# Optimization experiments

Measured on AMD Instinct MI355X. Metric: run time of the kernel, lower is better.

## Reference

```python
import jax, jax.numpy as jnp
import numpy as np

B, S = 16, 768
DCOG, DENV, NENV = 64, 32, 8
D, N, L, FF, NC = 512, 64, 6, 2048, 1
DIL = (1, 2, 4, 8)
EPS = 1e-5


def _layer_norm(x, g, b):
    m = x.mean(-1, keepdims=True)
    v = ((x - m) ** 2).mean(-1, keepdims=True)
    return (x - m) * jax.lax.rsqrt(v + EPS) * g + b


def _conv1d(x, w, b, d):
    # x: (B, D, S), w: (O, I, K); 'same' padding = (K-1)*d//2 = d for K=3
    y = jax.lax.conv_general_dilated(x, w, (1,), [(d, d)], rhs_dilation=(d,),
                                     dimension_numbers=('NCH', 'OIH', 'NCH'))
    return y + b[None, :, None]


def _combine(c1, c2):
    a1, b1 = c1
    a2, b2 = c2
    return a1 * a2, a2 * b1 + b2


def _forward(x_cog, cw1, cb1, cw2, cb2, env_emb, ew1, eb1, ew2, eb2,
             fw1, fb1, fw2, fb2, pos_enc, conv_w, conv_b, wm_w, wm_b,
             ssm_w, ssm_b, A_log, ffw1, ffb1, ffw2, ffb2,
             g1, be1, g2, be2, pw1, pb1, pw2, pb2, x_env):
    # Dual-channel feature processor (dropout = identity at eval)
    z = x_cog / jnp.maximum(jnp.linalg.norm(x_cog, axis=-1, keepdims=True), 1e-12)
    z = jnp.maximum(z @ cw1 + cb1, 0.0) @ cw2 + cb2
    e = env_emb[x_env].mean(-2)                      # (B,S,NENV,D) -> (B,S,D)
    e = jnp.maximum(e @ ew1 + eb1, 0.0) @ ew2 + eb2
    hf = jnp.concatenate([z, e], -1)
    hf = jnp.maximum(hf @ fw1 + fb1, 0.0) @ fw2 + fb2
    h = hf + pos_enc[:S][None]

    def layer_step(h, p):
        cw, cb, wmw, wmb, sw, sb, alog, w1, b1, w2, b2, g1_, be1_, g2_, be2_ = p
        # Multi-scale dilated conv
        xt = h.transpose(0, 2, 1)                    # (B, D, S)
        outs = [_conv1d(xt, cw[i], cb[i], DIL[i]) for i in range(4)]
        alpha = jax.nn.softmax(xt.mean(-1) @ wmw + wmb, -1)   # (B, 4)
        hm = sum(alpha[:, i, None, None] * outs[i] for i in range(4)).transpose(0, 2, 1)
        h1 = _layer_norm(hm + h, g1_, be1_)
        # Selective state-space (diagonal A), parallel associative scan
        proj = jnp.einsum('bsd,kdn->kbsn', h1, sw) + sb[:, None, None, :]
        delta, Bt, Ct = jax.nn.softplus(proj[0]), proj[1], proj[2]
        a = jnp.exp(alog[None, None, :] * delta)     # (B, S, N)
        bu = Bt * h1[..., :N]
        _, hs = jax.lax.associative_scan(_combine, (a, bu), axis=1)
        y = jnp.sum(Ct * hs, -1, keepdims=True)      # (B, S, 1)
        h2 = _layer_norm(y + h1, g2_, be2_)          # broadcast over D, as in torch
        return jnp.maximum(h2 @ w1 + b1, 0.0) @ w2 + b2 + h2, None

    h, _ = jax.lax.scan(layer_step, h, (conv_w, conv_b, wm_w, wm_b, ssm_w, ssm_b,
                                        A_log, ffw1, ffb1, ffw2, ffb2, g1, be1, g2, be2))
    hg = h.mean(1)                                   # adaptive avg pool over S
    return jnp.maximum(hg @ pw1 + pb1, 0.0) @ pw2 + pb2


def setup_inputs():
    ks = iter(jax.random.split(jax.random.key(0), 48))
    def rn(shape, s=0.02):
        return jax.random.normal(next(ks), shape, jnp.float32) * s
    return {
        'x_cog': rn((B, S, DCOG), 1.0),
        'cw1': rn((DCOG, D)), 'cb1': jnp.zeros(D), 'cw2': rn((D, D)), 'cb2': jnp.zeros(D),
        'env_emb': rn((DENV, D), 1.0),
        'ew1': rn((D, D)), 'eb1': jnp.zeros(D), 'ew2': rn((D, D)), 'eb2': jnp.zeros(D),
        'fw1': rn((2 * D, D)), 'fb1': jnp.zeros(D), 'fw2': rn((D, D)), 'fb2': jnp.zeros(D),
        'pos_enc': rn((1000, D), 1.0),
        'conv_w': rn((L, 4, D, D, 3)), 'conv_b': jnp.zeros((L, 4, D)),
        'wm_w': rn((L, D, 4)), 'wm_b': jnp.zeros((L, 4)),
        'ssm_w': rn((L, 3, D, N)), 'ssm_b': jnp.zeros((L, 3, N)),
        'A_log': -jnp.abs(rn((L, N), 1.0)),
        'ffw1': rn((L, D, FF)), 'ffb1': jnp.zeros((L, FF)),
        'ffw2': rn((L, FF, D)), 'ffb2': jnp.zeros((L, D)),
        'g1': jnp.ones((L, D)), 'be1': jnp.zeros((L, D)),
        'g2': jnp.ones((L, D)), 'be2': jnp.zeros((L, D)),
        'pw1': rn((D, D // 2)), 'pb1': jnp.zeros(D // 2),
        'pw2': rn((D // 2, NC)), 'pb2': jnp.zeros(NC),
        'x_env': jax.random.randint(next(ks), (B, S, NENV), 0, DENV, jnp.int32),
    }


def reference(x_cog, cw1, cb1, cw2, cb2, env_emb, ew1, eb1, ew2, eb2,
              fw1, fb1, fw2, fb2, pos_enc, conv_w, conv_b, wm_w, wm_b,
              ssm_w, ssm_b, A_log, ffw1, ffb1, ffw2, ffb2,
              g1, be1, g2, be2, pw1, pb1, pw2, pb2, x_env):
    return _forward(x_cog, cw1, cb1, cw2, cb2, env_emb, ew1, eb1, ew2, eb2,
                    fw1, fb1, fw2, fb2, pos_enc, conv_w, conv_b, wm_w, wm_b,
                    ssm_w, ssm_b, A_log, ffw1, ffb1, ffw2, ffb2,
                    g1, be1, g2, be2, pw1, pb1, pw2, pb2, x_env)
```

## Files before the change

### kernel.cpp

```cpp
#include <hip/hip_runtime.h>
#include <cstdint>
#include <cstddef>

namespace {

constexpr int B = 16, S = 768, BS = B * S, D = 512, FF = 2048, L = 6;
constexpr float EPS = 1e-5f;

typedef float f32x4 __attribute__((ext_vector_type(4)));
typedef _Float16 f16x8 __attribute__((ext_vector_type(8)));

__device__ __forceinline__ float wave_sum(float v) {
#pragma unroll
  for (int o = 32; o > 0; o >>= 1) v += __shfl_xor(v, o, 64);
  return v;
}

__device__ __forceinline__ short f16b(float x) {
  const _Float16 h = (_Float16)x;
  return __builtin_bit_cast(short, h);
}

__device__ __forceinline__ void gload16(const void* g, void* l) {
  __builtin_amdgcn_global_load_lds(
      (const __attribute__((address_space(1))) void*)g,
      (__attribute__((address_space(3))) void*)l, 16, 0, 0);
}


template <bool RELU, bool RESID, bool FOUT, bool PACK>
__global__ __launch_bounds__(256, 3) void gemm_h(
    const short* __restrict__ A, int lda, const short* __restrict__ Wt,
    int ldw, int Klen, const float* __restrict__ bias,
    const float* __restrict__ resid, int ldr, int rmod,
    float* __restrict__ fout, int ldc, short* __restrict__ ph, int ldp) {
  __shared__ alignas(16) short sAh[8192], sBh[8192];
  const int tid = threadIdx.x;
  const unsigned Nt = gridDim.x;
  const unsigned lin = blockIdx.y * Nt + blockIdx.x;
  const unsigned cpx = (Nt * gridDim.y) >> 3;
  const unsigned swz = (lin & 7) * cpx + (lin >> 3);
  const int bn = (int)(swz % Nt) * 128, bm = (int)(swz / Nt) * 128;
  const int wave = tid >> 6, lane = tid & 63;
  const int wr = (wave >> 1) * 64, wc = (wave & 1) * 64;
  const int lr = lane & 15, sl = lane >> 4;
  const short* Ab = A + (size_t)bm * lda;
  const short* Wb = Wt + (size_t)bn * ldw;
  f32x4 acc[4][4] = {};
  for (int kk = 0; kk < Klen; kk += 64) {
#pragma unroll
    for (int jj = 0; jj < 4; ++jj) {
      const int G = jj * 256 + tid;
      const int srow = G >> 3, sl0 = G & 7;
      const int gsl = sl0 ^ (srow & 7);
      const int dst = G * 8;
      gload16(Ab + (size_t)srow * lda + kk + gsl * 8, &sAh[dst]);
      gload16(Wb + (size_t)srow * ldw + kk + gsl * 8, &sBh[dst]);
    }
    __syncthreads();
#pragma unroll
    for (int ks = 0; ks < 2; ++ks) {
      f16x8 aH[4], bH[4];
#pragma unroll
      for (int m = 0; m < 4; ++m) {
        const int r = wr + m * 16 + lr;
        aH[m] = *(const f16x8*)&sAh[r * 64 + (((ks * 4 + sl) ^ (r & 7)) * 8)];
      }
#pragma unroll
      for (int n = 0; n < 4; ++n) {
        const int r = wc + n * 16 + lr;
        bH[n] = *(const f16x8*)&sBh[r * 64 + (((ks * 4 + sl) ^ (r & 7)) * 8)];
      }
#pragma unroll
      for (int m = 0; m < 4; ++m)
#pragma unroll
        for (int n = 0; n < 4; ++n)
          acc[m][n] = __builtin_amdgcn_mfma_f32_16x16x32_f16(aH[m], bH[n],
                                                             acc[m][n], 0, 0, 0);
    }
    __syncthreads();
  }
  const int r4 = sl * 4;
#pragma unroll
  for (int m = 0; m < 4; ++m) {
#pragma unroll
    for (int r = 0; r < 4; ++r) {
      const int mm = bm + wr + m * 16 + r4 + r;
#pragma unroll
      for (int n = 0; n < 4; ++n) {
        const int col = bn + wc + n * 16 + lr;
        float v = acc[m][n][r] + bias[col];
        if (RELU) v = fmaxf(v, 0.f);
        if (RESID) {
          const int rr = rmod ? (mm % rmod) : mm;
          v += resid[(size_t)rr * ldr + col];
        }
        if (FOUT) fout[(size_t)mm * ldc + col] = v;
        if (PACK) ph[(size_t)mm * ldp + col] = f16b(v);
      }
    }
  }
}

template <bool RELU, bool RESID, bool FOUT, bool PACK>
__global__ __launch_bounds__(256, 3) void gemm_h64(
    const short* __restrict__ A, int lda, const short* __restrict__ Wt,
    int ldw, int Klen, const float* __restrict__ bias,
    const float* __restrict__ resid, int ldr, int rmod,
    float* __restrict__ fout, int ldc, short* __restrict__ ph, int ldp) {
  __shared__ alignas(16) short sAh[8192], sBh[4096];
  const int tid = threadIdx.x;
  const unsigned Nt = gridDim.x;
  const unsigned lin = blockIdx.y * Nt + blockIdx.x;
  const unsigned cpx = (Nt * gridDim.y) >> 3;
  const unsigned swz = (lin & 7) * cpx + (lin >> 3);
  const int bn = (int)(swz % Nt) * 64, bm = (int)(swz / Nt) * 128;
  const int wave = tid >> 6, lane = tid & 63;
  const int wr = (wave >> 1) * 64, wc = (wave & 1) * 32;
  const int lr = lane & 15, sl = lane >> 4;
  const short* Ab = A + (size_t)bm * lda;
  const short* Wb = Wt + (size_t)bn * ldw;
  f32x4 acc[4][2] = {};
  for (int kk = 0; kk < Klen; kk += 64) {
#pragma unroll
    for (int jj = 0; jj < 4; ++jj) {
      const int G = jj * 256 + tid;
      const int srow = G >> 3, sl0 = G & 7;
      const int gsl = sl0 ^ (srow & 7);
      gload16(Ab + (size_t)srow * lda + kk + gsl * 8, &sAh[G * 8]);
    }
#pragma unroll
    for (int jj = 0; jj < 2; ++jj) {
      const int G = jj * 256 + tid;
      const int srow = G >> 3, sl0 = G & 7;
      const int gsl = sl0 ^ (srow & 7);
      gload16(Wb + (size_t)srow * ldw + kk + gsl * 8, &sBh[G * 8]);
    }
    __syncthreads();
#pragma unroll
    for (int ks = 0; ks < 2; ++ks) {
      f16x8 aH[4], bH[2];
#pragma unroll
      for (int m = 0; m < 4; ++m) {
        const int r = wr + m * 16 + lr;
        aH[m] = *(const f16x8*)&sAh[r * 64 + (((ks * 4 + sl) ^ (r & 7)) * 8)];
      }
#pragma unroll
      for (int n = 0; n < 2; ++n) {
        const int r = wc + n * 16 + lr;
        bH[n] = *(const f16x8*)&sBh[r * 64 + (((ks * 4 + sl) ^ (r & 7)) * 8)];
      }
#pragma unroll
      for (int m = 0; m < 4; ++m)
#pragma unroll
        for (int n = 0; n < 2; ++n)
          acc[m][n] = __builtin_amdgcn_mfma_f32_16x16x32_f16(aH[m], bH[n],
                                                             acc[m][n], 0, 0, 0);
    }
    __syncthreads();
  }
  const int r4 = sl * 4;
#pragma unroll
  for (int m = 0; m < 4; ++m) {
#pragma unroll
    for (int r = 0; r < 4; ++r) {
      const int mm = bm + wr + m * 16 + r4 + r;
#pragma unroll
      for (int n = 0; n < 2; ++n) {
        const int col = bn + wc + n * 16 + lr;
        float v = acc[m][n][r] + bias[col];
        if (RELU) v = fmaxf(v, 0.f);
        if (RESID) {
          const int rr = rmod ? (mm % rmod) : mm;
          v += resid[(size_t)rr * ldr + col];
        }
        if (FOUT) fout[(size_t)mm * ldc + col] = v;
        if (PACK) ph[(size_t)mm * ldp + col] = f16b(v);
      }
    }
  }
}

__global__ __launch_bounds__(256, 3) void conv_zp_k(
    const short* __restrict__ hp, const short* __restrict__ wt8,
    const short* __restrict__ wmix, const float* __restrict__ alpha,
    const short* __restrict__ zpadS, float* __restrict__ P) {
  __shared__ alignas(16) short sAh[8192], sBh[8192];
  const int tid = threadIdx.x;
  const unsigned lin = blockIdx.x;
  const unsigned swz = (lin & 7) * 96 + (lin >> 3);
  const int zp = (int)(swz / 384);
  const unsigned rem = swz % 384;
  const int bn = (int)(rem & 3) * 128;
  const int bmt = (int)(rem >> 2);
  const int b = bmt / 6, s0 = (bmt % 6) * 128, gm0 = bmt * 128;
  const int wave = tid >> 6, lane = tid & 63;
  const int wr = (wave >> 1) * 64, wc = (wave & 1) * 64;
  const int lr = lane & 15, sl = lane >> 4;
  const short* hb = hp + (size_t)b * S * 512;
  f32x4 accF[4][4] = {};
#pragma unroll
  for (int zi = 0; zi < 2; ++zi) {
    const int z = zp * 2 + zi;
    const int dd = 1 << z;
    f32x4 acc[4][4] = {};
    for (int kk = 0; kk < 1024; kk += 64) {
      const int tap = kk >> 9;
      const int koff = kk & 511;
      const int off = tap ? dd : -dd;
#pragma unroll
      for (int jj = 0; jj < 4; ++jj) {
        const int G = jj * 256 + tid;
        const int srow = G >> 3, sl0 = G & 7;
        const int gsl = sl0 ^ (srow & 7);
        const int dst = G * 8;
        const int gs = s0 + srow + off;
        const bool inb = ((unsigned)gs < (unsigned)S);
        const short* aBase = hb + (size_t)gs * 512 + koff + gsl * 8;
        gload16(inb ? aBase : zpadS, &sAh[dst]);
        gload16(wt8 + ((size_t)((z * 2 + tap) * 512 + bn + srow)) * 512 +
                    koff + gsl * 8,
                &sBh[dst]);
      }
      __syncthreads();
#pragma unroll
      for (int ks = 0; ks < 2; ++ks) {
        f16x8 aH[4], bH[4];
#pragma unroll
        for (int m = 0; m < 4; ++m) {
          const int r = wr + m * 16 + lr;
          aH[m] =
              *(const f16x8*)&sAh[r * 64 + (((ks * 4 + sl) ^ (r & 7)) * 8)];
        }
#pragma unroll
        for (int n = 0; n < 4; ++n) {
          const int r = wc + n * 16 + lr;
          bH[n] =
              *(const f16x8*)&sBh[r * 64 + (((ks * 4 + sl) ^ (r & 7)) * 8)];
        }
#pragma unroll
        for (int m = 0; m < 4; ++m)
#pragma unroll
          for (int n = 0; n < 4; ++n)
            acc[m][n] = __builtin_amdgcn_mfma_f32_16x16x32_f16(
                aH[m], bH[n], acc[m][n], 0, 0, 0);
      }
      __syncthreads();
    }
    const float al = alpha[b * 4 + z];
#pragma unroll
    for (int m = 0; m < 4; ++m)
#pragma unroll
      for (int n = 0; n < 4; ++n)
#pragma unroll
        for (int r = 0; r < 4; ++r) accF[m][n][r] += al * acc[m][n][r];
  }
  const short* Wm = wmix + (size_t)b * 512 * 512;
  for (int kc = 0; kc < 256; kc += 64) {
    const int koff = zp * 256 + kc;
#pragma unroll
    for (int jj = 0; jj < 4; ++jj) {
      const int G = jj * 256 + tid;
      const int srow = G >> 3, sl0 = G & 7;
      const int gsl = sl0 ^ (srow & 7);
      const int dst = G * 8;
      gload16(hb + (size_t)(s0 + srow) * 512 + koff + gsl * 8, &sAh[dst]);
      gload16(Wm + (size_t)(bn + srow) * 512 + koff + gsl * 8, &sBh[dst]);
    }
    __syncthreads();
#pragma unroll
    for (int ks = 0; ks < 2; ++ks) {
      f16x8 aH[4], bH[4];
#pragma unroll
      for (int m = 0; m < 4; ++m) {
        const int r = wr + m * 16 + lr;
        aH[m] = *(const f16x8*)&sAh[r * 64 + (((ks * 4 + sl) ^ (r & 7)) * 8)];
      }
#pragma unroll
      for (int n = 0; n < 4; ++n) {
        const int r = wc + n * 16 + lr;
        bH[n] = *(const f16x8*)&sBh[r * 64 + (((ks * 4 + sl) ^ (r & 7)) * 8)];
      }
#pragma unroll
      for (int m = 0; m < 4; ++m)
#pragma unroll
        for (int n = 0; n < 4; ++n)
          accF[m][n] = __builtin_amdgcn_mfma_f32_16x16x32_f16(
              aH[m], bH[n], accF[m][n], 0, 0, 0);
    }
    __syncthreads();
  }
  float* Pz = P + (size_t)zp * ((size_t)BS * D);
  const int r4 = sl * 4;
#pragma unroll
  for (int m = 0; m < 4; ++m)
#pragma unroll
    for (int r = 0; r < 4; ++r) {
      const int mm = gm0 + wr + m * 16 + r4 + r;
#pragma unroll
      for (int n = 0; n < 4; ++n)
        Pz[(size_t)mm * D + bn + wc + n * 16 + lr] = accF[m][n][r];
    }
}

__global__ __launch_bounds__(256) void ln3_k(
    const float* __restrict__ P0, const float* __restrict__ P1,
    const float* __restrict__ resid, const float* __restrict__ cbmix,
    const float* __restrict__ g1, const float* __restrict__ b1,
    const float* __restrict__ g2, const float* __restrict__ b2,
    float* __restrict__ fout, short* __restrict__ pout) {
  const int row = blockIdx.x * 4 + (threadIdx.x >> 6);
  const int lane = threadIdx.x & 63;
  const int bb = row / S;
  const size_t base = (size_t)row * D;
  float v[8];
  float s = 0.f;
#pragma unroll
  for (int j = 0; j < 8; ++j) {
    const int c = lane + 64 * j;
    v[j] = P0[base + c] + P1[base + c] + resid[base + c] +
           cbmix[(size_t)bb * D + c];
    s += v[j];
  }
  s = wave_sum(s);
  const float m1 = s * (1.f / D);
  float q = 0.f;
#pragma unroll
  for (int j = 0; j < 8; ++j) { const float d = v[j] - m1; q += d * d; }
  q = wave_sum(q);
  const float r1 = rsqrtf(q * (1.f / D) + EPS);
  float y[8];
  float s2 = 0.f;
#pragma unroll
  for (int j = 0; j < 8; ++j) {
    const int c = lane + 64 * j;
    y[j] = (v[j] - m1) * r1 * g1[c] + b1[c];
    s2 += y[j];
  }
  s2 = wave_sum(s2);
  const float m2 = s2 * (1.f / D);
  float q2 = 0.f;
#pragma unroll
  for (int j = 0; j < 8; ++j) { const float d = y[j] - m2; q2 += d * d; }
  q2 = wave_sum(q2);
  const float r2 = rsqrtf(q2 * (1.f / D) + EPS);
  float* frow = fout + base;
  short* prow = pout + (size_t)row * 512;
#pragma unroll
  for (int j = 0; j < 8; ++j) {
    const int c = lane + 64 * j;
    const float o = (y[j] - m2) * r2 * g2[c] + b2[c];
    frow[c] = o;
    prow[c] = f16b(o);
  }
}

__global__ __launch_bounds__(256) void colmean_part_k(
    const float* __restrict__ x, float* __restrict__ part) {
  const int b = blockIdx.x, c = blockIdx.y;
  const int s0 = c * 96;
  for (int d = threadIdx.x; d < D; d += 256) {
    float s = 0.f;
    for (int si = 0; si < 96; ++si)
      s += x[((size_t)b * S + s0 + si) * D + d];
    part[((size_t)b * 8 + c) * D + d] = s;
  }
}

__global__ __launch_bounds__(256) void pack_wh_k(const float* __restrict__ W,
                                                 short* __restrict__ out,
                                                 int K, int N, int ln2N) {
  const int idx = blockIdx.x * 256 + threadIdx.x;
  const int n = idx & (N - 1), k = idx >> ln2N;
  if (k >= K) return;
  out[(size_t)n * K + k] = f16b(W[(size_t)k * N + n]);
}

__global__ __launch_bounds__(256) void pack_convw8_k(
    const float* __restrict__ cw, short* __restrict__ out) {
  const int idx = blockIdx.x * 256 + threadIdx.x;
  const int c = idx & 511, o = (idx >> 9) & 511, seg = idx >> 18;
  const int z = seg >> 1, t = (seg & 1) * 2;
  out[((size_t)seg * D + o) * D + c] =
      f16b(cw[(((size_t)z * D + o) * D + c) * 3 + t]);
}

__global__ __launch_bounds__(256) void wmix_k(const float* __restrict__ cw,
                                              const float* __restrict__ alpha,
                                              short* __restrict__ wm) {
  __shared__ float sal[64];
  if (threadIdx.x < 64) sal[threadIdx.x] = alpha[threadIdx.x];
  __syncthreads();
  const int idx = blockIdx.x * 256 + threadIdx.x;
  const int c = idx & 511, o = idx >> 9;
  float w[4];
#pragma unroll
  for (int z = 0; z < 4; ++z)
    w[z] = cw[(((size_t)z * D + o) * D + c) * 3 + 1];
#pragma unroll
  for (int b = 0; b < 16; ++b) {
    const float v = sal[b * 4 + 0] * w[0] + sal[b * 4 + 1] * w[1] +
                    sal[b * 4 + 2] * w[2] + sal[b * 4 + 3] * w[3];
    wm[((size_t)b * D + o) * D + c] = f16b(v);
  }
}

__global__ __launch_bounds__(256) void zero_k(float* __restrict__ p) {
  p[threadIdx.x] = 0.f;
  p[threadIdx.x + 256] = 0.f;
}

__global__ __launch_bounds__(64) void alpha_k(const float* __restrict__ part,
                                              const float* __restrict__ wmw,
                                              const float* __restrict__ wmb,
                                              const float* __restrict__ cb,
                                              float* __restrict__ alpha,
                                              float* __restrict__ cbmix) {
  const int b = blockIdx.x, t = threadIdx.x;
  float p0 = 0, p1 = 0, p2 = 0, p3 = 0;
  for (int d = t; d < D; d += 64) {
    float xm = 0;
#pragma unroll
    for (int c = 0; c < 8; ++c) xm += part[((size_t)b * 8 + c) * D + d];
    xm *= (1.f / S);
    p0 += xm * wmw[d * 4 + 0];
    p1 += xm * wmw[d * 4 + 1];
    p2 += xm * wmw[d * 4 + 2];
    p3 += xm * wmw[d * 4 + 3];
  }
  p0 = wave_sum(p0); p1 = wave_sum(p1);
  p2 = wave_sum(p2); p3 = wave_sum(p3);
  const float l0 = p0 + wmb[0], l1 = p1 + wmb[1];
  const float l2 = p2 + wmb[2], l3 = p3 + wmb[3];
  const float mx = fmaxf(fmaxf(l0, l1), fmaxf(l2, l3));
  const float e0 = expf(l0 - mx), e1 = expf(l1 - mx);
  const float e2 = expf(l2 - mx), e3 = expf(l3 - mx);
  const float inv = 1.f / (e0 + e1 + e2 + e3);
  const float a0 = e0 * inv, a1 = e1 * inv, a2 = e2 * inv, a3 = e3 * inv;
  if (t == 0) {
    alpha[b * 4 + 0] = a0;
    alpha[b * 4 + 1] = a1;
    alpha[b * 4 + 2] = a2;
    alpha[b * 4 + 3] = a3;
  }
  for (int c = t; c < D; c += 64)
    cbmix[(size_t)b * D + c] =
        a0 * cb[c] + a1 * cb[D + c] + a2 * cb[2 * D + c] + a3 * cb[3 * D + c];
}

__global__ __launch_bounds__(256) void embed_k(const int* __restrict__ xe,
                                               const float* __restrict__ emb,
                                               short* __restrict__ out) {
  const int r = blockIdx.x;
  int idx[8];
#pragma unroll
  for (int j = 0; j < 8; ++j) idx[j] = xe[r * 8 + j];
  short* o = out + (size_t)r * 512;
  for (int d = threadIdx.x; d < D; d += 256) {
    float s = 0.f;
#pragma unroll
    for (int j = 0; j < 8; ++j) s += emb[(size_t)idx[j] * D + d];
    o[d] = f16b(s * 0.125f);
  }
}

__global__ __launch_bounds__(256) void norml2_k(const float* __restrict__ x,
                                                short* __restrict__ out) {
  const int r = blockIdx.x * 4 + (threadIdx.x >> 6);
  const int lane = threadIdx.x & 63;
  const float v = x[(size_t)r * 64 + lane];
  const float s = wave_sum(v * v);
  const float nrm = fmaxf(sqrtf(s), 1e-12f);
  out[(size_t)r * 64 + lane] = f16b(v / nrm);
}

__global__ __launch_bounds__(256) void head_k(
    const float* __restrict__ part, const float* __restrict__ pw1,
    const float* __restrict__ pb1, const float* __restrict__ pw2,
    const float* __restrict__ pb2, float* __restrict__ out) {
  __shared__ float hg[D];
  __shared__ float red[256];
  const int b = blockIdx.x, t = threadIdx.x;
  for (int d = t; d < D; d += 256) {
    float s = 0.f;
#pragma unroll
    for (int c = 0; c < 8; ++c) s += part[((size_t)b * 8 + c) * D + d];
    hg[d] = s * (1.f / S);
  }
  __syncthreads();
  float s = pb1[t];
  for (int d = 0; d < D; ++d) s = fmaf(hg[d], pw1[(size_t)d * 256 + t], s);
  s = fmaxf(s, 0.f);
  red[t] = s * pw2[t];
  __syncthreads();
  for (int o = 128; o > 0; o >>= 1) {
    if (t < o) red[t] += red[t + o];
    __syncthreads();
  }
  if (t == 0) out[b] = red[0] + pb2[0];
}

}

extern "C" void kernel_launch(void* const* d_in, const int* in_sizes, int n_in,
                              void* d_out, int out_size, void* d_ws,
                              size_t ws_size, hipStream_t stream) {
  const float* x_cog = (const float*)d_in[0];
  const float* cw1 = (const float*)d_in[1];
  const float* cb1 = (const float*)d_in[2];
  const float* cw2 = (const float*)d_in[3];
  const float* cb2 = (const float*)d_in[4];
  const float* env_emb = (const float*)d_in[5];
  const float* ew1 = (const float*)d_in[6];
  const float* eb1 = (const float*)d_in[7];
  const float* ew2 = (const float*)d_in[8];
  const float* eb2 = (const float*)d_in[9];
  const float* fw1 = (const float*)d_in[10];
  const float* fb1 = (const float*)d_in[11];
  const float* fw2 = (const float*)d_in[12];
  const float* fb2 = (const float*)d_in[13];
  const float* pos_enc = (const float*)d_in[14];
  const float* conv_w = (const float*)d_in[15];
  const float* conv_b = (const float*)d_in[16];
  const float* wm_w = (const float*)d_in[17];
  const float* wm_b = (const float*)d_in[18];
  const float* ffw1 = (const float*)d_in[22];
  const float* ffb1 = (const float*)d_in[23];
  const float* ffw2 = (const float*)d_in[24];
  const float* ffb2 = (const float*)d_in[25];
  const float* g1 = (const float*)d_in[26];
  const float* be1 = (const float*)d_in[27];
  const float* g2 = (const float*)d_in[28];
  const float* be2 = (const float*)d_in[29];
  const float* pw1 = (const float*)d_in[30];
  const float* pb1 = (const float*)d_in[31];
  const float* pw2 = (const float*)d_in[32];
  const float* pb2 = (const float*)d_in[33];
  const int* x_env = (const int*)d_in[34];
  float* out = (float*)d_out;

  float* ws = (float*)d_ws;
  float* Hbuf = ws;
  float* TBuf = Hbuf + 6291456;
  float* PARTb = TBuf + 6291456;
  float* ALPHAB = PARTb + 65536;
  float* ZPADF = ALPHAB + 64;
  float* CBMIX = ZPADF + 512;
  short* R = (short*)(CBMIX + 8192);
  short* CONC = R;
  short* PK1 = R + 25165824;
  short* PK2 = R + 31457280;
  short* WPBF = R + 37748736;
  short* WCONV8 = R;
  short* WFFP = R + 2097152;
  short* WMIX = R + 3145728;
  float* convP = (float*)(R + 7340032);
  short* APFF = R + 7340032;
  short* HPACK = R + 57671680;

  const dim3 blk(256);
  const dim3 gS(8, 96, 1);
  const dim3 gF(16, 96, 1);

  zero_k<<<1, blk, 0, stream>>>(ZPADF);

  norml2_k<<<BS / 4, blk, 0, stream>>>(x_cog, PK1);
  pack_wh_k<<<64 * 512 / 256, blk, 0, stream>>>(cw1, WPBF, 64, 512, 9);
  gemm_h64<true, false, false, true><<<gS, blk, 0, stream>>>(
      PK1, 64, WPBF, 64, 64, cb1, nullptr, 0, 0, nullptr, 0, PK2, 512);
  pack_wh_k<<<512 * 512 / 256, blk, 0, stream>>>(cw2, WPBF, 512, 512, 9);
  gemm_h64<false, false, false, true><<<gS, blk, 0, stream>>>(
      PK2, 512, WPBF, 512, 512, cb2, nullptr, 0, 0, nullptr, 0, CONC, 2048);
  embed_k<<<BS, blk, 0, stream>>>(x_env, env_emb, PK1);
  pack_wh_k<<<512 * 512 / 256, blk, 0, stream>>>(ew1, WPBF, 512, 512, 9);
  gemm_h64<true, false, false, true><<<gS, blk, 0, stream>>>(
      PK1, 512, WPBF, 512, 512, eb1, nullptr, 0, 0, nullptr, 0, PK2, 512);
  pack_wh_k<<<512 * 512 / 256, blk, 0, stream>>>(ew2, WPBF, 512, 512, 9);
  gemm_h64<false, false, false, true><<<gS, blk, 0, stream>>>(
      PK2, 512, WPBF, 512, 512, eb2, nullptr, 0, 0, nullptr, 0, CONC + 512,
      2048);
  pack_wh_k<<<1024 * 512 / 256, blk, 0, stream>>>(fw1, WPBF, 1024, 512, 9);
  gemm_h64<true, false, false, true><<<gS, blk, 0, stream>>>(
      CONC, 2048, WPBF, 1024, 1024, fb1, nullptr, 0, 0, nullptr, 0, PK1, 512);
  pack_wh_k<<<512 * 512 / 256, blk, 0, stream>>>(fw2, WPBF, 512, 512, 9);
  gemm_h64<false, true, true, true><<<gS, blk, 0, stream>>>(
      PK1, 512, WPBF, 512, 512, fb2, pos_enc, 512, S, Hbuf, 512, HPACK, 512);

  for (int l = 0; l < L; ++l) {
    const float* cwl = conv_w + (size_t)l * 4 * D * D * 3;
    colmean_part_k<<<dim3(B, 8), blk, 0, stream>>>(Hbuf, PARTb);
    alpha_k<<<B, dim3(64), 0, stream>>>(PARTb, wm_w + (size_t)l * D * 4,
                                        wm_b + l * 4,
                                        conv_b + (size_t)l * 4 * D, ALPHAB,
                                        CBMIX);
    wmix_k<<<1024, blk, 0, stream>>>(cwl, ALPHAB, WMIX);
    pack_convw8_k<<<8 * 512 * 512 / 256, blk, 0, stream>>>(cwl, WCONV8);
    conv_zp_k<<<768, blk, 0, stream>>>(HPACK, WCONV8, WMIX, ALPHAB,
                                       (const short*)ZPADF, convP);
    ln3_k<<<BS / 4, blk, 0, stream>>>(convP, convP + 6291456, Hbuf, CBMIX,
                                      g1 + l * D, be1 + l * D, g2 + l * D,
                                      be2 + l * D, TBuf, HPACK);
    pack_wh_k<<<512 * 2048 / 256, blk, 0, stream>>>(ffw1 + (size_t)l * D * FF,
                                                    WFFP, 512, 2048, 11);
    gemm_h<true, false, false, true><<<gF, blk, 0, stream>>>(
        HPACK, 512, WFFP, 512, 512, ffb1 + (size_t)l * FF, nullptr, 0, 0,
        nullptr, 0, APFF, 2048);
    pack_wh_k<<<2048 * 512 / 256, blk, 0, stream>>>(ffw2 + (size_t)l * FF * D,
                                                    WFFP, 2048, 512, 9);
    gemm_h64<false, true, true, true><<<gS, blk, 0, stream>>>(
        APFF, 2048, WFFP, 2048, 2048, ffb2 + (size_t)l * D, TBuf, 512, 0,
        Hbuf, 512, HPACK, 512);
  }

  colmean_part_k<<<dim3(B, 8), blk, 0, stream>>>(Hbuf, PARTb);
  head_k<<<B, blk, 0, stream>>>(PARTb, pw1, pb1, pw2, pb2, out);
}
```

Before: 1.376 ms.

## Fuse column sums into GEMM epilogue, fp16 conv partials, tiled weight packing

The separate colmean kernel is removed. The D-dimension column sums of each 128-row tile are now produced in the epilogue of the FF2/fusion GEMMs, and alpha/head read 6 partials per batch. The conv partial outputs are stored as fp16 instead of fp32, halving that round-trip traffic at some precision cost. Weight transposition now goes through an LDS tile so both reads and writes are coalesced. The two conv weight prep kernels are merged into one launch, and the workspace layout is reshuffled to fit.

```diff
diff --git a/kernel.cpp b/kernel.cpp
--- a/kernel.cpp
+++ b/kernel.cpp
@@ -19,6 +19,9 @@
 __device__ __forceinline__ short f16b(float x) {
   const _Float16 h = (_Float16)x;
   return __builtin_bit_cast(short, h);
+}
+__device__ __forceinline__ float h2f(short s) {
+  return (float)__builtin_bit_cast(_Float16, s);
 }
 
 __device__ __forceinline__ void gload16(const void* g, void* l) {
@@ -102,19 +105,22 @@
   }
 }
 
-template <bool RELU, bool RESID, bool FOUT, bool PACK>
+template <bool RELU, bool RESID, bool FOUT, bool PACK, bool CSUM>
 __global__ __launch_bounds__(256, 3) void gemm_h64(
     const short* __restrict__ A, int lda, const short* __restrict__ Wt,
     int ldw, int Klen, const float* __restrict__ bias,
     const float* __restrict__ resid, int ldr, int rmod,
-    float* __restrict__ fout, int ldc, short* __restrict__ ph, int ldp) {
+    float* __restrict__ fout, int ldc, short* __restrict__ ph, int ldp,
+    float* __restrict__ part) {
   __shared__ alignas(16) short sAh[8192], sBh[4096];
+  __shared__ float csLds[2][64];
   const int tid = threadIdx.x;
   const unsigned Nt = gridDim.x;
   const unsigned lin = blockIdx.y * Nt + blockIdx.x;
   const unsigned cpx = (Nt * gridDim.y) >> 3;
   const unsigned swz = (lin & 7) * cpx + (lin >> 3);
-  const int bn = (int)(swz % Nt) * 64, bm = (int)(swz / Nt) * 128;
+  const int bn = (int)(swz % Nt) * 64, bmt = (int)(swz / Nt);
+  const int bm = bmt * 128;
   const int wave = tid >> 6, lane = tid & 63;
   const int wr = (wave >> 1) * 64, wc = (wave & 1) * 32;
   const int lr = lane & 15, sl = lane >> 4;
@@ -160,6 +166,7 @@
     __syncthreads();
   }
   const int r4 = sl * 4;
+  float cs[2] = {0.f, 0.f};
 #pragma unroll
   for (int m = 0; m < 4; ++m) {
 #pragma unroll
@@ -176,15 +183,30 @@
         }
         if (FOUT) fout[(size_t)mm * ldc + col] = v;
         if (PACK) ph[(size_t)mm * ldp + col] = f16b(v);
-      }
-    }
+        if (CSUM) cs[n] += v;
+      }
+    }
+  }
+  if constexpr (CSUM) {
+#pragma unroll
+    for (int n = 0; n < 2; ++n) {
+      cs[n] += __shfl_xor(cs[n], 16, 64);
+      cs[n] += __shfl_xor(cs[n], 32, 64);
+    }
+    if (sl == 0) {
+      csLds[wave >> 1][wc + lr] = cs[0];
+      csLds[wave >> 1][wc + 16 + lr] = cs[1];
+    }
+    __syncthreads();
+    if (tid < 64)
+      part[(size_t)bmt * 512 + bn + tid] = csLds[0][tid] + csLds[1][tid];
   }
 }
 
 __global__ __launch_bounds__(256, 3) void conv_zp_k(
     const short* __restrict__ hp, const short* __restrict__ wt8,
     const short* __restrict__ wmix, const float* __restrict__ alpha,
-    const short* __restrict__ zpadS, float* __restrict__ P) {
+    const short* __restrict__ zpadS, short* __restrict__ P) {
   __shared__ alignas(16) short sAh[8192], sBh[8192];
   const int tid = threadIdx.x;
   const unsigned lin = blockIdx.x;
@@ -290,7 +312,7 @@
     }
     __syncthreads();
   }
-  float* Pz = P + (size_t)zp * ((size_t)BS * D);
+  short* Pz = P + (size_t)zp * ((size_t)BS * D);
   const int r4 = sl * 4;
 #pragma unroll
   for (int m = 0; m < 4; ++m)
@@ -299,12 +321,12 @@
       const int mm = gm0 + wr + m * 16 + r4 + r;
 #pragma unroll
       for (int n = 0; n < 4; ++n)
-        Pz[(size_t)mm * D + bn + wc + n * 16 + lr] = accF[m][n][r];
+        Pz[(size_t)mm * D + bn + wc + n * 16 + lr] = f16b(accF[m][n][r]);
     }
 }
 
 __global__ __launch_bounds__(256) void ln3_k(
-    const float* __restrict__ P0, const float* __restrict__ P1,
+    const short* __restrict__ P0, const short* __restrict__ P1,
     const float* __restrict__ resid, const float* __restrict__ cbmix,
     const float* __restrict__ g1, const float* __restrict__ b1,
     const float* __restrict__ g2, const float* __restrict__ b2,
@@ -318,7 +340,7 @@
 #pragma unroll
   for (int j = 0; j < 8; ++j) {
     const int c = lane + 64 * j;
-    v[j] = P0[base + c] + P1[base + c] + resid[base + c] +
+    v[j] = h2f(P0[base + c]) + h2f(P1[base + c]) + resid[base + c] +
            cbmix[(size_t)bb * D + c];
     s += v[j];
   }
@@ -355,53 +377,51 @@
   }
 }
 
-__global__ __launch_bounds__(256) void colmean_part_k(
-    const float* __restrict__ x, float* __restrict__ part) {
-  const int b = blockIdx.x, c = blockIdx.y;
-  const int s0 = c * 96;
-  for (int d = threadIdx.x; d < D; d += 256) {
-    float s = 0.f;
-    for (int si = 0; si < 96; ++si)
-      s += x[((size_t)b * S + s0 + si) * D + d];
-    part[((size_t)b * 8 + c) * D + d] = s;
-  }
-}
-
-__global__ __launch_bounds__(256) void pack_wh_k(const float* __restrict__ W,
+__global__ __launch_bounds__(256) void pack_wt_k(const float* __restrict__ W,
                                                  short* __restrict__ out,
-                                                 int K, int N, int ln2N) {
-  const int idx = blockIdx.x * 256 + threadIdx.x;
-  const int n = idx & (N - 1), k = idx >> ln2N;
-  if (k >= K) return;
-  out[(size_t)n * K + k] = f16b(W[(size_t)k * N + n]);
-}
-
-__global__ __launch_bounds__(256) void pack_convw8_k(
-    const float* __restrict__ cw, short* __restrict__ out) {
-  const int idx = blockIdx.x * 256 + threadIdx.x;
-  const int c = idx & 511, o = (idx >> 9) & 511, seg = idx >> 18;
-  const int z = seg >> 1, t = (seg & 1) * 2;
-  out[((size_t)seg * D + o) * D + c] =
-      f16b(cw[(((size_t)z * D + o) * D + c) * 3 + t]);
-}
-
-__global__ __launch_bounds__(256) void wmix_k(const float* __restrict__ cw,
-                                              const float* __restrict__ alpha,
-                                              short* __restrict__ wm) {
-  __shared__ float sal[64];
-  if (threadIdx.x < 64) sal[threadIdx.x] = alpha[threadIdx.x];
+                                                 int K, int N) {
+  __shared__ short t[64][68];
+  const int n0 = blockIdx.x * 64, k0 = blockIdx.y * 64;
+  const int ln = threadIdx.x & 63, w4 = threadIdx.x >> 6;
+#pragma unroll
+  for (int it = 0; it < 16; ++it) {
+    const int kr = it * 4 + w4;
+    t[kr][ln] = f16b(W[(size_t)(k0 + kr) * N + n0 + ln]);
+  }
   __syncthreads();
-  const int idx = blockIdx.x * 256 + threadIdx.x;
-  const int c = idx & 511, o = idx >> 9;
-  float w[4];
-#pragma unroll
-  for (int z = 0; z < 4; ++z)
-    w[z] = cw[(((size_t)z * D + o) * D + c) * 3 + 1];
-#pragma unroll
-  for (int b = 0; b < 16; ++b) {
-    const float v = sal[b * 4 + 0] * w[0] + sal[b * 4 + 1] * w[1] +
-                    sal[b * 4 + 2] * w[2] + sal[b * 4 + 3] * w[3];
-    wm[((size_t)b * D + o) * D + c] = f16b(v);
+#pragma unroll
+  for (int it = 0; it < 16; ++it) {
+    const int nr = it * 4 + w4;
+    out[(size_t)(n0 + nr) * K + k0 + ln] = t[ln][nr];
+  }
+}
+
+__global__ __launch_bounds__(256) void convprep_k(
+    const float* __restrict__ cw, const float* __restrict__ alpha,
+    short* __restrict__ out8, short* __restrict__ wm) {
+  const int bid = blockIdx.x;
+  if (bid < 8192) {
+    const int idx = bid * 256 + threadIdx.x;
+    const int c = idx & 511, o = (idx >> 9) & 511, seg = idx >> 18;
+    const int z = seg >> 1, t = (seg & 1) * 2;
+    out8[((size_t)seg * D + o) * D + c] =
+        f16b(cw[(((size_t)z * D + o) * D + c) * 3 + t]);
+  } else {
+    __shared__ float sal[64];
+    if (threadIdx.x < 64) sal[threadIdx.x] = alpha[threadIdx.x];
+    __syncthreads();
+    const int idx = (bid - 8192) * 256 + threadIdx.x;
+    const int c = idx & 511, o = idx >> 9;
+    float w[4];
+#pragma unroll
+    for (int z = 0; z < 4; ++z)
+      w[z] = cw[(((size_t)z * D + o) * D + c) * 3 + 1];
+#pragma unroll
+    for (int b = 0; b < 16; ++b) {
+      const float v = sal[b * 4 + 0] * w[0] + sal[b * 4 + 1] * w[1] +
+                      sal[b * 4 + 2] * w[2] + sal[b * 4 + 3] * w[3];
+      wm[((size_t)b * D + o) * D + c] = f16b(v);
+    }
   }
 }
 
@@ -421,7 +441,7 @@
   for (int d = t; d < D; d += 64) {
     float xm = 0;
 #pragma unroll
-    for (int c = 0; c < 8; ++c) xm += part[((size_t)b * 8 + c) * D + d];
+    for (int c = 0; c < 6; ++c) xm += part[((size_t)(b * 6 + c)) * D + d];
     xm *= (1.f / S);
     p0 += xm * wmw[d * 4 + 0];
     p1 += xm * wmw[d * 4 + 1];
@@ -484,7 +504,7 @@
   for (int d = t; d < D; d += 256) {
     float s = 0.f;
 #pragma unroll
-    for (int c = 0; c < 8; ++c) s += part[((size_t)b * 8 + c) * D + d];
+    for (int c = 0; c < 6; ++c) s += part[((size_t)(b * 6 + c)) * D + d];
     hg[d] = s * (1.f / S);
   }
   __syncthreads();
@@ -542,21 +562,21 @@
   float* ws = (float*)d_ws;
   float* Hbuf = ws;
   float* TBuf = Hbuf + 6291456;
-  float* PARTb = TBuf + 6291456;
-  float* ALPHAB = PARTb + 65536;
+  float* PART2 = TBuf + 6291456;
+  float* ALPHAB = PART2 + 65536;
   float* ZPADF = ALPHAB + 64;
   float* CBMIX = ZPADF + 512;
   short* R = (short*)(CBMIX + 8192);
-  short* CONC = R;
-  short* PK1 = R + 25165824;
-  short* PK2 = R + 31457280;
-  short* WPBF = R + 37748736;
   short* WCONV8 = R;
   short* WFFP = R + 2097152;
   short* WMIX = R + 3145728;
-  float* convP = (float*)(R + 7340032);
+  short* convPh = R + 7340032;
   short* APFF = R + 7340032;
-  short* HPACK = R + 57671680;
+  short* HPACK = R + 32505856;
+  short* CONC = R;
+  short* PK1 = R + 25165824;
+  short* PK2 = R + 25165824 + 6291456;
+  short* WPBF = WFFP;
 
   const dim3 blk(256);
   const dim3 gS(8, 96, 1);
@@ -565,53 +585,55 @@
   zero_k<<<1, blk, 0, stream>>>(ZPADF);
 
   norml2_k<<<BS / 4, blk, 0, stream>>>(x_cog, PK1);
-  pack_wh_k<<<64 * 512 / 256, blk, 0, stream>>>(cw1, WPBF, 64, 512, 9);
-  gemm_h64<true, false, false, true><<<gS, blk, 0, stream>>>(
-      PK1, 64, WPBF, 64, 64, cb1, nullptr, 0, 0, nullptr, 0, PK2, 512);
-  pack_wh_k<<<512 * 512 / 256, blk, 0, stream>>>(cw2, WPBF, 512, 512, 9);
-  gemm_h64<false, false, false, true><<<gS, blk, 0, stream>>>(
-      PK2, 512, WPBF, 512, 512, cb2, nullptr, 0, 0, nullptr, 0, CONC, 2048);
+  pack_wt_k<<<dim3(8, 1), blk, 0, stream>>>(cw1, WPBF, 64, 512);
+  gemm_h64<true, false, false, true, false><<<gS, blk, 0, stream>>>(
+      PK1, 64, WPBF, 64, 64, cb1, nullptr, 0, 0, nullptr, 0, PK2, 512,
+      nullptr);
+  pack_wt_k<<<dim3(8, 8), blk, 0, stream>>>(cw2, WPBF, 512, 512);
+  gemm_h64<false, false, false, true, false><<<gS, blk, 0, stream>>>(
+      PK2, 512, WPBF, 512, 512, cb2, nullptr, 0, 0, nullptr, 0, CONC, 2048,
+      nullptr);
   embed_k<<<BS, blk, 0, stream>>>(x_env, env_emb, PK1);
-  pack_wh_k<<<512 * 512 / 256, blk, 0, stream>>>(ew1, WPBF, 512, 512, 9);
-  gemm_h64<true, false, false, true><<<gS, blk, 0, stream>>>(
-      PK1, 512, WPBF, 512, 512, eb1, nullptr, 0, 0, nullptr, 0, PK2, 512);
-  pack_wh_k<<<512 * 512 / 256, blk, 0, stream>>>(ew2, WPBF, 512, 512, 9);
-  gemm_h64<false, false, false, true><<<gS, blk, 0, stream>>>(
+  pack_wt_k<<<dim3(8, 8), blk, 0, stream>>>(ew1, WPBF, 512, 512);
+  gemm_h64<true, false, false, true, false><<<gS, blk, 0, stream>>>(
+      PK1, 512, WPBF, 512, 512, eb1, nullptr, 0, 0, nullptr, 0, PK2, 512,
+      nullptr);
+  pack_wt_k<<<dim3(8, 8), blk, 0, stream>>>(ew2, WPBF, 512, 512);
+  gemm_h64<false, false, false, true, false><<<gS, blk, 0, stream>>>(
       PK2, 512, WPBF, 512, 512, eb2, nullptr, 0, 0, nullptr, 0, CONC + 512,
-      2048);
-  pack_wh_k<<<1024 * 512 / 256, blk, 0, stream>>>(fw1, WPBF, 1024, 512, 9);
-  gemm_h64<true, false, false, true><<<gS, blk, 0, stream>>>(
-      CONC, 2048, WPBF, 1024, 1024, fb1, nullptr, 0, 0, nullptr, 0, PK1, 512);
-  pack_wh_k<<<512 * 512 / 256, blk, 0, stream>>>(fw2, WPBF, 512, 512, 9);
-  gemm_h64<false, true, true, true><<<gS, blk, 0, stream>>>(
-      PK1, 512, WPBF, 512, 512, fb2, pos_enc, 512, S, Hbuf, 512, HPACK, 512);
+      2048, nullptr);
+  pack_wt_k<<<dim3(8, 16), blk, 0, stream>>>(fw1, WPBF, 1024, 512);
+  gemm_h64<true, false, false, true, false><<<gS, blk, 0, stream>>>(
+      CONC, 2048, WPBF, 1024, 1024, fb1, nullptr, 0, 0, nullptr, 0, PK1, 512,
+      nullptr);
+  pack_wt_k<<<dim3(8, 8), blk, 0, stream>>>(fw2, WPBF, 512, 512);
+  gemm_h64<false, true, true, true, true><<<gS, blk, 0, stream>>>(
+      PK1, 512, WPBF, 512, 512, fb2, pos_enc, 512, S, Hbuf, 512, HPACK, 512,
+      PART2);
 
   for (int l = 0; l < L; ++l) {
     const float* cwl = conv_w + (size_t)l * 4 * D * D * 3;
-    colmean_part_k<<<dim3(B, 8), blk, 0, stream>>>(Hbuf, PARTb);
-    alpha_k<<<B, dim3(64), 0, stream>>>(PARTb, wm_w + (size_t)l * D * 4,
+    alpha_k<<<B, dim3(64), 0, stream>>>(PART2, wm_w + (size_t)l * D * 4,
                                         wm_b + l * 4,
                                         conv_b + (size_t)l * 4 * D, ALPHAB,
                                         CBMIX);
-    wmix_k<<<1024, blk, 0, stream>>>(cwl, ALPHAB, WMIX);
-    pack_convw8_k<<<8 * 512 * 512 / 256, blk, 0, stream>>>(cwl, WCONV8);
+    convprep_k<<<9216, blk, 0, stream>>>(cwl, ALPHAB, WCONV8, WMIX);
     conv_zp_k<<<768, blk, 0, stream>>>(HPACK, WCONV8, WMIX, ALPHAB,
-                                       (const short*)ZPADF, convP);
-    ln3_k<<<BS / 4, blk, 0, stream>>>(convP, convP + 6291456, Hbuf, CBMIX,
-                                      g1 + l * D, be1 + l * D, g2 + l * D,
-                                      be2 + l * D, TBuf, HPACK);
-    pack_wh_k<<<512 * 2048 / 256, blk, 0, stream>>>(ffw1 + (size_t)l * D * FF,
-                                                    WFFP, 512, 2048, 11);
+                                       (const short*)ZPADF, convPh);
+    ln3_k<<<BS / 4, blk, 0, stream>>>(convPh, convPh + (size_t)BS * D, Hbuf,
+                                      CBMIX, g1 + l * D, be1 + l * D,
+                                      g2 + l * D, be2 + l * D, TBuf, HPACK);
+    pack_wt_k<<<dim3(32, 8), blk, 0, stream>>>(ffw1 + (size_t)l * D * FF,
+                                               WFFP, 512, 2048);
     gemm_h<true, false, false, true><<<gF, blk, 0, stream>>>(
         HPACK, 512, WFFP, 512, 512, ffb1 + (size_t)l * FF, nullptr, 0, 0,
         nullptr, 0, APFF, 2048);
-    pack_wh_k<<<2048 * 512 / 256, blk, 0, stream>>>(ffw2 + (size_t)l * FF * D,
-                                                    WFFP, 2048, 512, 9);
-    gemm_h64<false, true, true, true><<<gS, blk, 0, stream>>>(
+    pack_wt_k<<<dim3(8, 32), blk, 0, stream>>>(ffw2 + (size_t)l * FF * D,
+                                               WFFP, 2048, 512);
+    gemm_h64<false, true, true, true, true><<<gS, blk, 0, stream>>>(
         APFF, 2048, WFFP, 2048, 2048, ffb2 + (size_t)l * D, TBuf, 512, 0,
-        Hbuf, 512, HPACK, 512);
-  }
-
-  colmean_part_k<<<dim3(B, 8), blk, 0, stream>>>(Hbuf, PARTb);
-  head_k<<<B, blk, 0, stream>>>(PARTb, pw1, pb1, pw2, pb2, out);
-}
+        Hbuf, 512, HPACK, 512, PART2);
+  }
+
+  head_k<<<B, blk, 0, stream>>>(PART2, pw1, pb1, pw2, pb2, out);
+}
```

After: 1.212 ms. 12.0% less time.
